# Kernel optimization log

Measured on AMD Instinct MI355X. Metric: run time of the kernel, lower is better.

The kernel has to match this reference:

```python
import jax, jax.numpy as jnp
import numpy as np

IN_DIM = 1024
HID = 2048
BATCH = 8192


def setup_inputs() -> dict:
    key = jax.random.key(0)
    ks = jax.random.split(key, 10)
    s1 = 1.0 / np.sqrt(IN_DIM)
    s2 = 1.0 / np.sqrt(HID)
    inp = {
        "x": jax.random.normal(ks[0], (BATCH, IN_DIM), dtype=jnp.float32),
        "W1": jax.random.uniform(ks[1], (IN_DIM, HID), jnp.float32, -s1, s1),
        "b1": jax.random.uniform(ks[2], (HID,), jnp.float32, -s1, s1),
        "W2": jax.random.uniform(ks[3], (HID, HID), jnp.float32, -s2, s2),
        "b2": jax.random.uniform(ks[4], (HID,), jnp.float32, -s2, s2),
        "W3": jax.random.uniform(ks[5], (HID, HID), jnp.float32, -s2, s2),
        "b3": jax.random.uniform(ks[6], (HID,), jnp.float32, -s2, s2),
        "Wout": jax.random.uniform(ks[7], (HID, 1), jnp.float32, -s2, s2),
        "bout": jax.random.uniform(ks[8], (1,), jnp.float32, -s2, s2),
        "weight": jnp.array([0.1], dtype=jnp.float32),
        "bias": jnp.array([0.0], dtype=jnp.float32),
        "scale": jnp.array([1.0], dtype=jnp.float32),
        "shift": jnp.array([0.0], dtype=jnp.float32),
    }
    return inp


def reference(x, W1, b1, W2, b2, W3, b3, Wout, bout, weight, bias, scale, shift):
    # 3-layer tanh MLP core
    h = jnp.tanh(x @ W1 + b1)
    h = jnp.tanh(h @ W2 + b2)
    core_out = jnp.tanh(h @ W3 + b3)  # [B, HID]
    # Closed form of per-element 1-qubit statevector sim:
    # <Y> for RX(w) RY(v) H |0>  ==  sin(w) * sin(v)
    q_out = jnp.sin(weight[0]) * jnp.sin(core_out)
    q_out = (q_out + bias[0]) * scale[0] + shift[0]
    out = core_out + q_out
    out = out @ Wout + bout  # [B, 1]
    return out.squeeze(-1)  # [B]
```

## Files before the change

### kernel.cpp

```cpp
#include <hip/hip_runtime.h>
#include <hip/hip_bf16.h>


typedef _Float16 f16;
typedef __attribute__((ext_vector_type(8))) _Float16 f16x8;
typedef __attribute__((ext_vector_type(4))) _Float16 f16x4;
typedef __attribute__((ext_vector_type(4))) float f32x4;

#define BATCH 8192
#define IN_DIM 1024
#define HID 2048

__device__ __forceinline__ float fast_tanh(float x) {
  x = fminf(12.0f, fmaxf(-12.0f, x));
  float e = __expf(2.0f * x);
  return (e - 1.0f) * __builtin_amdgcn_rcpf(e + 1.0f);
}

__global__ __launch_bounds__(256) void cast_kernel(const float* __restrict__ in,
                                                   f16* __restrict__ out, int n4) {
  int i = blockIdx.x * blockDim.x + threadIdx.x;
  if (i < n4) {
    float4 v = reinterpret_cast<const float4*>(in)[i];
    f16x4 o = { (f16)v.x, (f16)v.y, (f16)v.z, (f16)v.w };
    reinterpret_cast<f16x4*>(out)[i] = o;
  }
}

__global__ __launch_bounds__(256) void transpose_cast3(
    const float* __restrict__ W1, const float* __restrict__ W2,
    const float* __restrict__ W3, f16* __restrict__ w1t,
    f16* __restrict__ w2t, f16* __restrict__ w3t) {
  __shared__ float tile[32][33];
  int b = blockIdx.x;
  const float* W; f16* Wt; int K, N;
  if (b < 2048)      { W = W1; Wt = w1t; K = IN_DIM; N = HID; }
  else if (b < 6144) { W = W2; Wt = w2t; K = HID;    N = HID; b -= 2048; }
  else               { W = W3; Wt = w3t; K = HID;    N = HID; b -= 6144; }
  const int nbt = N / 32;
  const int nb = (b % nbt) * 32, kb = (b / nbt) * 32;
  const int tx = threadIdx.x, ty = threadIdx.y;
#pragma unroll
  for (int i = 0; i < 4; ++i)
    tile[ty + i * 8][tx] = W[(size_t)(kb + ty + i * 8) * N + nb + tx];
  __syncthreads();
#pragma unroll
  for (int i = 0; i < 4; ++i)
    Wt[(size_t)(nb + ty + i * 8) * K + kb + tx] = (f16)tile[tx][ty + i * 8];
}


#define GLDS16(g, l)                                                         \
  __builtin_amdgcn_global_load_lds(                                          \
      (const __attribute__((address_space(1))) unsigned int*)(g),            \
      (__attribute__((address_space(3))) unsigned int*)(l), 16, 0, 0)

template <int K>
__global__ __launch_bounds__(512, 2) void gemm256_bias_tanh(
    const f16* __restrict__ A,
    const f16* __restrict__ Bt,
    const float* __restrict__ bias,
    f16* __restrict__ Out) {
  constexpr int NT = K / 32;
  __shared__ f16 smem[65536];
  f16* As = smem;
  f16* Bs = smem + 32768;

  const int T = threadIdx.x;
  const int l = T & 63;
  const int w = T >> 6;
  const int wm = w >> 2, wn = w & 3;
  const int lr = l & 15;
  const int lc = l >> 4;

  const int bm = (int)blockIdx.x >> 3;
  const int bn = (int)blockIdx.x & 7;
  const int tm = bm << 8, tn = bn << 8;

  const int srow = ((T >> 5) << 3) + (T & 7);
  const int skel = ((T >> 3) & 3) << 3;
  const f16* gA0 = A + (size_t)(tm + srow) * K + skel;
  const f16* gA1 = A + (size_t)(tm + srow + 128) * K + skel;
  const f16* gB0 = Bt + (size_t)(tn + srow) * K + skel;
  const f16* gB1 = Bt + (size_t)(tn + srow + 128) * K + skel;
  const int ldsw0 = w * 512;
  const int ldsw1 = 4096 + w * 512;

  const int abase = (wm * 16 + (lr >> 3)) * 256 + lc * 64 + (lr & 7) * 8;
  const int bbase = (wn * 8 + (lr >> 3)) * 256 + lc * 64 + (lr & 7) * 8;

  f32x4 acc[8][4] = {};

#pragma unroll
  for (int p = 0; p < 3; ++p) {
    const int ko = p * 32;
    f16* aq = As + p * 8192;
    f16* bq = Bs + p * 8192;
    GLDS16(gA0 + ko, aq + ldsw0);
    GLDS16(gA1 + ko, aq + ldsw1);
    GLDS16(gB0 + ko, bq + ldsw0);
    GLDS16(gB1 + ko, bq + ldsw1);
  }
  asm volatile("s_waitcnt vmcnt(8)" ::: "memory");
  __builtin_amdgcn_s_barrier();
  __builtin_amdgcn_sched_barrier(0);

  for (int t = 0; t < NT; ++t) {
    const int q = t & 3;
    const f16* aq = As + q * 8192;
    const f16* bq = Bs + q * 8192;
    f16x8 afr[8], bfr[4];
#pragma unroll
    for (int mi = 0; mi < 8; ++mi)
      afr[mi] = *reinterpret_cast<const f16x8*>(&aq[abase + mi * 512]);
#pragma unroll
    for (int ni = 0; ni < 4; ++ni)
      bfr[ni] = *reinterpret_cast<const f16x8*>(&bq[bbase + ni * 512]);
    if (t + 3 < NT) {
      const int q3 = (t + 3) & 3;
      const int ko = (t + 3) * 32;
      f16* aw = As + q3 * 8192;
      f16* bw = Bs + q3 * 8192;
      GLDS16(gA0 + ko, aw + ldsw0);
      GLDS16(gA1 + ko, aw + ldsw1);
      GLDS16(gB0 + ko, bw + ldsw0);
      GLDS16(gB1 + ko, bw + ldsw1);
    }
    __builtin_amdgcn_s_setprio(1);
#pragma unroll
    for (int mi = 0; mi < 8; ++mi)
#pragma unroll
      for (int ni = 0; ni < 4; ++ni)
        acc[mi][ni] = __builtin_amdgcn_mfma_f32_16x16x32_f16(
            afr[mi], bfr[ni], acc[mi][ni], 0, 0, 0);
    __builtin_amdgcn_s_setprio(0);
    if (t + 3 < NT) {
      asm volatile("s_waitcnt vmcnt(8)" ::: "memory");
    } else if (t + 2 < NT) {
      asm volatile("s_waitcnt vmcnt(4)" ::: "memory");
    } else {
      asm volatile("s_waitcnt vmcnt(0)" ::: "memory");
    }
    __builtin_amdgcn_s_barrier();
    __builtin_amdgcn_sched_barrier(0);
  }

#pragma unroll
  for (int ni = 0; ni < 4; ++ni) {
    const int col = wn * 64 + ni * 16 + lr;
    const float bv = bias[tn + col];
#pragma unroll
    for (int mi = 0; mi < 8; ++mi) {
      const int r0 = wm * 128 + mi * 16 + ((l >> 4) << 2);
#pragma unroll
      for (int j = 0; j < 4; ++j) {
        const int r = r0 + j;
        const int bo = r * 512 + ((col * 2) ^ ((r & 7) << 4));
        *reinterpret_cast<f16*>(reinterpret_cast<char*>(smem) + bo) =
            (f16)fast_tanh(acc[mi][ni][j] + bv);
      }
    }
  }
  __syncthreads();
#pragma unroll
  for (int it = 0; it < 16; ++it) {
    const int r = w * 32 + it * 2 + (l >> 5);
    const int cb = (l & 31) * 16;
    const int so = r * 512 + (cb ^ ((r & 7) << 4));
    f16x8 v = *reinterpret_cast<const f16x8*>(
        reinterpret_cast<const char*>(smem) + so);
    *reinterpret_cast<f16x8*>(
        reinterpret_cast<char*>(Out + (size_t)(tm + r) * HID + tn) + cb) = v;
  }
}

__global__ __launch_bounds__(256) void final_reduce(
    const f16* __restrict__ core, const float* __restrict__ Wout,
    const float* __restrict__ bout, const float* __restrict__ weight,
    const float* __restrict__ qbias, const float* __restrict__ qscale,
    const float* __restrict__ qshift, float* __restrict__ out) {
  const int b = blockIdx.x, t = threadIdx.x;
  const float sw = __sinf(weight[0]);
  const float qb = qbias[0], qs = qscale[0], qsh = qshift[0];
  f16x8 c8 = *reinterpret_cast<const f16x8*>(&core[(size_t)b * HID + t * 8]);
  float sum = 0.f;
#pragma unroll
  for (int j = 0; j < 8; ++j) {
    float c = (float)c8[j];
    float s = c + (sw * __sinf(c) + qb) * qs + qsh;
    sum += s * Wout[t * 8 + j];
  }
#pragma unroll
  for (int off = 32; off >= 1; off >>= 1) sum += __shfl_down(sum, off, 64);
  __shared__ float red[4];
  if ((t & 63) == 0) red[t >> 6] = sum;
  __syncthreads();
  if (t == 0) out[b] = red[0] + red[1] + red[2] + red[3] + bout[0];
}

extern "C" void kernel_launch(void* const* d_in, const int* in_sizes, int n_in,
                              void* d_out, int out_size, void* d_ws, size_t ws_size,
                              hipStream_t stream) {
  const float* x    = (const float*)d_in[0];
  const float* W1   = (const float*)d_in[1];
  const float* b1   = (const float*)d_in[2];
  const float* W2   = (const float*)d_in[3];
  const float* b2   = (const float*)d_in[4];
  const float* W3   = (const float*)d_in[5];
  const float* b3   = (const float*)d_in[6];
  const float* Wout = (const float*)d_in[7];
  const float* bout = (const float*)d_in[8];
  const float* wgt  = (const float*)d_in[9];
  const float* qb   = (const float*)d_in[10];
  const float* qs   = (const float*)d_in[11];
  const float* qsh  = (const float*)d_in[12];
  float* out = (float*)d_out;

  char* ws = (char*)d_ws;
  size_t off = 0;
  f16* xh  = (f16*)(ws + off); off += (size_t)BATCH * IN_DIM * sizeof(f16);
  f16* w1t = (f16*)(ws + off); off += (size_t)HID * IN_DIM * sizeof(f16);
  f16* w2t = (f16*)(ws + off); off += (size_t)HID * HID * sizeof(f16);
  f16* w3t = (f16*)(ws + off); off += (size_t)HID * HID * sizeof(f16);
  f16* h1  = (f16*)(ws + off); off += (size_t)BATCH * HID * sizeof(f16);
  f16* h2  = (f16*)(ws + off); off += (size_t)BATCH * HID * sizeof(f16);

  {
    int n4 = BATCH * IN_DIM / 4;
    cast_kernel<<<(n4 + 255) / 256, 256, 0, stream>>>(x, xh, n4);
  }
  {
    dim3 blk(32, 8);
    transpose_cast3<<<10240, blk, 0, stream>>>(W1, W2, W3, w1t, w2t, w3t);
  }
  const int grid = (BATCH / 256) * (HID / 256);
  gemm256_bias_tanh<IN_DIM><<<grid, 512, 0, stream>>>(xh, w1t, b1, h1);
  gemm256_bias_tanh<HID>   <<<grid, 512, 0, stream>>>(h1, w2t, b2, h2);
  gemm256_bias_tanh<HID>   <<<grid, 512, 0, stream>>>(h2, w3t, b3, h1);
  final_reduce<<<BATCH, 256, 0, stream>>>(h1, Wout, bout, wgt, qb, qs, qsh, out);
}
```

Measured before the change: 332.6 us.

## Restructure GEMM main loop into double-buffered 64-wide K tiles with interleaved phases

```diff
diff --git a/kernel.cpp b/kernel.cpp
--- a/kernel.cpp
+++ b/kernel.cpp
@@ -61,89 +61,126 @@
     const f16* __restrict__ Bt,
     const float* __restrict__ bias,
     f16* __restrict__ Out) {
-  constexpr int NT = K / 32;
+  constexpr int NT = K / 64;
   __shared__ f16 smem[65536];
-  f16* As = smem;
-  f16* Bs = smem + 32768;
 
   const int T = threadIdx.x;
   const int l = T & 63;
   const int w = T >> 6;
   const int wm = w >> 2, wn = w & 3;
-  const int lr = l & 15;
-  const int lc = l >> 4;
+  const int lr = l & 15, lc = l >> 4;
 
   const int bm = (int)blockIdx.x >> 3;
   const int bn = (int)blockIdx.x & 7;
   const int tm = bm << 8, tn = bn << 8;
 
-  const int srow = ((T >> 5) << 3) + (T & 7);
-  const int skel = ((T >> 3) & 3) << 3;
-  const f16* gA0 = A + (size_t)(tm + srow) * K + skel;
-  const f16* gA1 = A + (size_t)(tm + srow + 128) * K + skel;
-  const f16* gB0 = Bt + (size_t)(tn + srow) * K + skel;
-  const f16* gB1 = Bt + (size_t)(tn + srow + 128) * K + skel;
-  const int ldsw0 = w * 512;
-  const int ldsw1 = 4096 + w * 512;
-
   const int abase = (wm * 16 + (lr >> 3)) * 256 + lc * 64 + (lr & 7) * 8;
   const int bbase = (wn * 8 + (lr >> 3)) * 256 + lc * 64 + (lr & 7) * 8;
 
+  const int ccA0 = wm * 512 + wn * 128 + l;
+  const int ccA1 = ccA0 + 64;
+  const int ccB0 = (wn >> 1) * 512 + (wm * 2 + (wn & 1)) * 128 + l;
+  const int ccB1 = ccB0 + 64;
+#define ROWOF(cc) ((((cc) >> 5) << 3) | ((cc) & 7))
+#define KLOF(cc) ((((cc) >> 3) & 3) * 8)
+  const f16* pa0 = A + (size_t)(tm + ROWOF(ccA0)) * K + KLOF(ccA0);
+  const f16* pa1 = A + (size_t)(tm + ROWOF(ccA1)) * K + KLOF(ccA1);
+  const f16* pb0 = Bt + (size_t)(tn + ROWOF(ccB0)) * K + KLOF(ccB0);
+  const f16* pb1 = Bt + (size_t)(tn + ROWOF(ccB1)) * K + KLOF(ccB1);
+  const int dA = wm * 4096 + wn * 1024;
+  const int dB = 32768 + (wn >> 1) * 4096 + (wm * 2 + (wn & 1)) * 1024;
+
+#define STAGE_A(tt, u)                                                       \
+  do {                                                                       \
+    const int _b = ((tt) & 1) * 16384 + (u) * 8192;                          \
+    GLDS16(pa0 + (tt) * 64 + (u) * 32, &smem[_b + dA]);                      \
+    GLDS16(pa1 + (tt) * 64 + (u) * 32, &smem[_b + dA + 512]);                \
+  } while (0)
+#define STAGE_B(tt, u)                                                       \
+  do {                                                                       \
+    const int _b = ((tt) & 1) * 16384 + (u) * 8192;                          \
+    GLDS16(pb0 + (tt) * 64 + (u) * 32, &smem[_b + dB]);                      \
+    GLDS16(pb1 + (tt) * 64 + (u) * 32, &smem[_b + dB + 512]);                \
+  } while (0)
+#define LDF(p) (*reinterpret_cast<const f16x8*>(p))
+#define MFMA4(base)                                                          \
+  _Pragma("unroll") for (int mi = 0; mi < 4; ++mi)                           \
+  _Pragma("unroll") for (int ni = 0; ni < 4; ++ni)                           \
+      acc[(base) + mi][ni] = __builtin_amdgcn_mfma_f32_16x16x32_f16(         \
+          afr[mi], bfr[ni], acc[(base) + mi][ni], 0, 0, 0);
+
   f32x4 acc[8][4] = {};
 
-#pragma unroll
-  for (int p = 0; p < 3; ++p) {
-    const int ko = p * 32;
-    f16* aq = As + p * 8192;
-    f16* bq = Bs + p * 8192;
-    GLDS16(gA0 + ko, aq + ldsw0);
-    GLDS16(gA1 + ko, aq + ldsw1);
-    GLDS16(gB0 + ko, bq + ldsw0);
-    GLDS16(gB1 + ko, bq + ldsw1);
-  }
-  asm volatile("s_waitcnt vmcnt(8)" ::: "memory");
+  STAGE_A(0, 0); STAGE_B(0, 0); STAGE_A(0, 1); STAGE_B(0, 1);
+  asm volatile("s_waitcnt vmcnt(4)" ::: "memory");
   __builtin_amdgcn_s_barrier();
-  __builtin_amdgcn_sched_barrier(0);
 
   for (int t = 0; t < NT; ++t) {
-    const int q = t & 3;
-    const f16* aq = As + q * 8192;
-    const f16* bq = Bs + q * 8192;
-    f16x8 afr[8], bfr[4];
-#pragma unroll
-    for (int mi = 0; mi < 8; ++mi)
-      afr[mi] = *reinterpret_cast<const f16x8*>(&aq[abase + mi * 512]);
-#pragma unroll
-    for (int ni = 0; ni < 4; ++ni)
-      bfr[ni] = *reinterpret_cast<const f16x8*>(&bq[bbase + ni * 512]);
-    if (t + 3 < NT) {
-      const int q3 = (t + 3) & 3;
-      const int ko = (t + 3) * 32;
-      f16* aw = As + q3 * 8192;
-      f16* bw = Bs + q3 * 8192;
-      GLDS16(gA0 + ko, aw + ldsw0);
-      GLDS16(gA1 + ko, aw + ldsw1);
-      GLDS16(gB0 + ko, bw + ldsw0);
-      GLDS16(gB1 + ko, bw + ldsw1);
-    }
-    __builtin_amdgcn_s_setprio(1);
-#pragma unroll
-    for (int mi = 0; mi < 8; ++mi)
-#pragma unroll
-      for (int ni = 0; ni < 4; ++ni)
-        acc[mi][ni] = __builtin_amdgcn_mfma_f32_16x16x32_f16(
-            afr[mi], bfr[ni], acc[mi][ni], 0, 0, 0);
-    __builtin_amdgcn_s_setprio(0);
-    if (t + 3 < NT) {
-      asm volatile("s_waitcnt vmcnt(8)" ::: "memory");
-    } else if (t + 2 < NT) {
+    const int bo = (t & 1) * 16384;
+    const f16* As0 = smem + bo;
+    const f16* As1 = smem + bo + 8192;
+    const f16* Bs0 = smem + 32768 + bo;
+    const f16* Bs1 = smem + 32768 + bo + 8192;
+    f16x8 afr[4], bfr[4];
+
+#pragma unroll
+    for (int ni = 0; ni < 4; ++ni) bfr[ni] = LDF(Bs0 + bbase + ni * 512);
+#pragma unroll
+    for (int mi = 0; mi < 4; ++mi) afr[mi] = LDF(As0 + abase + mi * 512);
+    if (t + 1 < NT) STAGE_A(t + 1, 0);
+    __builtin_amdgcn_s_barrier();
+    asm volatile("s_waitcnt lgkmcnt(0)" ::: "memory");
+    __builtin_amdgcn_sched_barrier(0);
+    __builtin_amdgcn_s_setprio(1);
+    MFMA4(0)
+    __builtin_amdgcn_s_setprio(0);
+    __builtin_amdgcn_s_barrier();
+
+#pragma unroll
+    for (int mi = 0; mi < 4; ++mi) afr[mi] = LDF(As0 + abase + (4 + mi) * 512);
+    if (t + 1 < NT) STAGE_B(t + 1, 0);
+    __builtin_amdgcn_s_barrier();
+    asm volatile("s_waitcnt lgkmcnt(0)" ::: "memory");
+    __builtin_amdgcn_sched_barrier(0);
+    __builtin_amdgcn_s_setprio(1);
+    MFMA4(4)
+    __builtin_amdgcn_s_setprio(0);
+    if (t + 1 < NT) {
       asm volatile("s_waitcnt vmcnt(4)" ::: "memory");
     } else {
       asm volatile("s_waitcnt vmcnt(0)" ::: "memory");
     }
     __builtin_amdgcn_s_barrier();
-    __builtin_amdgcn_sched_barrier(0);
-  }
+
+#pragma unroll
+    for (int ni = 0; ni < 4; ++ni) bfr[ni] = LDF(Bs1 + bbase + ni * 512);
+#pragma unroll
+    for (int mi = 0; mi < 4; ++mi) afr[mi] = LDF(As1 + abase + mi * 512);
+    if (t + 1 < NT) STAGE_A(t + 1, 1);
+    __builtin_amdgcn_s_barrier();
+    asm volatile("s_waitcnt lgkmcnt(0)" ::: "memory");
+    __builtin_amdgcn_sched_barrier(0);
+    __builtin_amdgcn_s_setprio(1);
+    MFMA4(0)
+    __builtin_amdgcn_s_setprio(0);
+    __builtin_amdgcn_s_barrier();
+
+#pragma unroll
+    for (int mi = 0; mi < 4; ++mi) afr[mi] = LDF(As1 + abase + (4 + mi) * 512);
+    if (t + 1 < NT) STAGE_B(t + 1, 1);
+    __builtin_amdgcn_s_barrier();
+    asm volatile("s_waitcnt lgkmcnt(0)" ::: "memory");
+    __builtin_amdgcn_sched_barrier(0);
+    __builtin_amdgcn_s_setprio(1);
+    MFMA4(4)
+    __builtin_amdgcn_s_setprio(0);
+    if (t + 1 < NT) {
+      asm volatile("s_waitcnt vmcnt(4)" ::: "memory");
+    }
+    __builtin_amdgcn_s_barrier();
+  }
+
+  __syncthreads();
 
 #pragma unroll
   for (int ni = 0; ni < 4; ++ni) {
@@ -155,8 +192,8 @@
 #pragma unroll
       for (int j = 0; j < 4; ++j) {
         const int r = r0 + j;
-        const int bo = r * 512 + ((col * 2) ^ ((r & 7) << 4));
-        *reinterpret_cast<f16*>(reinterpret_cast<char*>(smem) + bo) =
+        const int bo2 = r * 512 + ((col * 2) ^ ((r & 7) << 4));
+        *reinterpret_cast<f16*>(reinterpret_cast<char*>(smem) + bo2) =
             (f16)fast_tanh(acc[mi][ni][j] + bv);
       }
     }
@@ -172,6 +209,12 @@
     *reinterpret_cast<f16x8*>(
         reinterpret_cast<char*>(Out + (size_t)(tm + r) * HID + tn) + cb) = v;
   }
+#undef STAGE_A
+#undef STAGE_B
+#undef LDF
+#undef MFMA4
+#undef ROWOF
+#undef KLOF
 }
 
 __global__ __launch_bounds__(256) void final_reduce(
```

Result: no change. 328.3 us (-1.3%).
